# Kernel optimization log

Hardware: AMD Instinct MI355X
Metric: run time of the kernel (lower is better)

Reference implementation:

```python
import jax, jax.numpy as jnp
import numpy as np

N = 4_194_304
L = 15
SLOPE = 0.01  # torch LeakyReLU default


def setup_inputs() -> dict:
    key = jax.random.key(0)
    ks = jax.random.split(key, 16)
    n = jax.random.normal
    return {
        "x": n(ks[0], (N, 2), jnp.float32),
        # scale Linear(1,1) per layer (small init keeps exp(log_scale) stable)
        "scale_w": n(ks[1], (L, 1, 1), jnp.float32) * 0.2,
        "scale_b": n(ks[2], (L, 1), jnp.float32) * 0.1,
        # g_theta_scale: 1->32->16->1
        "sW1": n(ks[3], (L, 1, 32), jnp.float32) * 0.5,
        "sb1": n(ks[4], (L, 32), jnp.float32) * 0.1,
        "sW2": n(ks[5], (L, 32, 16), jnp.float32) * 0.2,
        "sb2": n(ks[6], (L, 16), jnp.float32) * 0.1,
        "sW3": n(ks[7], (L, 16, 1), jnp.float32) * 0.2,
        "sb3": n(ks[8], (L, 1), jnp.float32) * 0.1,
        # g_theta_shift: 1->32->16->1
        "tW1": n(ks[9], (L, 1, 32), jnp.float32) * 0.5,
        "tb1": n(ks[10], (L, 32), jnp.float32) * 0.1,
        "tW2": n(ks[11], (L, 32, 16), jnp.float32) * 0.2,
        "tb2": n(ks[12], (L, 16), jnp.float32) * 0.1,
        "tW3": n(ks[13], (L, 16, 1), jnp.float32) * 0.2,
        "tb3": n(ks[14], (L, 1), jnp.float32) * 0.1,
    }


def _mlp(h, W1, b1, W2, b2, W3, b3):
    h = jax.nn.leaky_relu(h @ W1 + b1, SLOPE)
    h = jax.nn.leaky_relu(h @ W2 + b2, SLOPE)
    return h @ W3 + b3


def reference(x, scale_w, scale_b, sW1, sb1, sW2, sb2, sW3, sb3,
              tW1, tb1, tW2, tb2, tW3, tb3):
    def step(carry, p):
        z1, z2, ld = carry
        sw, sb, w1, b1, w2, b2, w3, b3, u1, c1, u2, c2, u3, c3 = p
        x1, x2 = z2, z1  # swap
        log_scale = jnp.tanh(_mlp(x1, w1, b1, w2, b2, w3, b3)) @ sw + sb
        z2n = jnp.exp(log_scale) * x2 + _mlp(x1, u1, c1, u2, c2, u3, c3)
        return (x1, z2n, ld + log_scale), None

    init = (x[:, 1:2], x[:, 0:1], jnp.zeros_like(x[:, :1]))
    params = (scale_w, scale_b, sW1, sb1, sW2, sb2, sW3, sb3,
              tW1, tb1, tW2, tb2, tW3, tb3)
    (z1, z2, ld), _ = jax.lax.scan(step, init, params)
    return jnp.concatenate((z1, z2), axis=1), ld
```

## Files before the change

kernel.cpp:

```cpp
#include <hip/hip_runtime.h>
#include <math.h>

#define SLOPE 0.01f
#define NLAYER 15
#define FINE_CELLS 512
#define COARSE_CELLS 128
#define CELLS 640
#define FINE_NODES 513
#define NODES_PER_NET 642
#define INV_LN2 1.4426950408889634f
#define LN2F 0.6931471805599453f
#define TPB 512
#define PAIRS 4

__device__ __forceinline__ float fast_exp2(float x) {
#if __has_builtin(__builtin_amdgcn_exp2f)
    return __builtin_amdgcn_exp2f(x);
#else
    return __expf(x * LN2F);
#endif
}

__device__ __forceinline__ float mlp_exact(
    float x1,
    const float* __restrict__ W1, const float* __restrict__ b1,
    const float* __restrict__ W2, const float* __restrict__ b2,
    const float* __restrict__ W3, float b3)
{
    float h2[16];
#pragma unroll
    for (int n = 0; n < 16; ++n) h2[n] = b2[n];
#pragma unroll 2
    for (int j = 0; j < 32; ++j) {
        float h = fmaf(W1[j], x1, b1[j]);
        h = fmaxf(h, SLOPE * h);
#pragma unroll
        for (int n = 0; n < 16; ++n) h2[n] = fmaf(h, W2[j * 16 + n], h2[n]);
    }
    float o = b3;
#pragma unroll
    for (int n = 0; n < 16; ++n) {
        float h = fmaxf(h2[n], SLOPE * h2[n]);
        o = fmaf(h, W3[n], o);
    }
    return o;
}

__global__ __launch_bounds__(640) void build_tables(
    const float* __restrict__ scale_w, const float* __restrict__ scale_b,
    const float* __restrict__ sW1, const float* __restrict__ sb1,
    const float* __restrict__ sW2, const float* __restrict__ sb2,
    const float* __restrict__ sW3, const float* __restrict__ sb3,
    const float* __restrict__ tW1, const float* __restrict__ tb1,
    const float* __restrict__ tW2, const float* __restrict__ tb2,
    const float* __restrict__ tW3, const float* __restrict__ tb3,
    float* __restrict__ ws)
{
    const int m = blockIdx.x;
    const int l = m >> 1;
    const int which = m & 1;
    const float* W1 = (which ? tW1 : sW1) + l * 32;
    const float* b1 = (which ? tb1 : sb1) + l * 32;
    const float* W2 = (which ? tW2 : sW2) + l * 512;
    const float* b2 = (which ? tb2 : sb2) + l * 16;
    const float* W3 = (which ? tW3 : sW3) + l * 16;
    const float  b3 = which ? tb3[l] : sb3[l];

    __shared__ float nodes[NODES_PER_NET];

    for (int i = threadIdx.x; i < NODES_PER_NET; i += blockDim.x) {
        const float x = (i < FINE_NODES) ? (-2.0f + (float)i * (1.0f / 128.0f))
                                         : (-32.0f + (float)(i - FINE_NODES) * 0.5f);
        float o = mlp_exact(x, W1, b1, W2, b2, W3, b3);
        nodes[i] = which ? o : fmaf(tanhf(o), scale_w[l], scale_b[l]) * INV_LN2;
    }
    __syncthreads();

    for (int c = threadIdx.x; c < CELLS; c += blockDim.x) {
        int base; float x_lo, invh;
        if (c < FINE_CELLS) { base = c;     x_lo = -2.0f  + (float)c * (1.0f / 128.0f); invh = 128.0f; }
        else                { base = c + 1; x_lo = -32.0f + (float)(c - FINE_CELLS) * 0.5f; invh = 2.0f; }
        float lo = nodes[base], hi = nodes[base + 1];
        float slope = (hi - lo) * invh;
        float icpt  = fmaf(-slope, x_lo, lo);
        *(float2*)(ws + ((size_t)(l * CELLS + c) * 4) + which * 2) = make_float2(slope, icpt);
    }
}

__device__ __forceinline__ int cell_index(float x) {
    float uf = fmaf(x, 128.0f, 256.0f);
    float uc = fmaf(x, 2.0f, 576.0f);
    bool fine = (fabsf(x) < 2.0f);
    float fu = fine ? floorf(uf)
                    : fminf(fmaxf(floorf(uc), 512.0f), 639.0f);
    return (int)fu;
}

__device__ __forceinline__ void couple(const float4* __restrict__ T,
                                       float& z1, float& z2, float& ld)
{
    float4 c = T[cell_index(z2)];
    float ls = fmaf(c.x, z2, c.y);
    float g  = fmaf(c.z, z2, c.w);
    float z2n = fmaf(fast_exp2(ls), z1, g);
    z1 = z2; z2 = z2n; ld += ls;
}

__global__ __launch_bounds__(TPB) void flow_lut(
    const float4* __restrict__ x,
    const float4* __restrict__ ws,
    float4* __restrict__ out_z,
    float2* __restrict__ out_ld,
    int npair)
{
    __shared__ __align__(16) float4 buf[2][CELLS];
    const int nthreads = gridDim.x * blockDim.x;
    const int tid0 = blockIdx.x * blockDim.x + threadIdx.x;

    for (int i = threadIdx.x; i < CELLS; i += TPB) buf[0][i] = ws[i];

    float az1[PAIRS], az2[PAIRS], ald[PAIRS];
    float bz1[PAIRS], bz2[PAIRS], bld[PAIRS];
#pragma unroll
    for (int k = 0; k < PAIRS; ++k) {
        int p = tid0 + k * nthreads;
        float4 xi = (p < npair) ? x[p] : make_float4(0.f, 0.f, 0.f, 0.f);
        az1[k] = xi.y; az2[k] = xi.x; ald[k] = 0.f;
        bz1[k] = xi.w; bz2[k] = xi.z; bld[k] = 0.f;
    }
    __syncthreads();

#pragma unroll
    for (int l = 0; l < NLAYER; ++l) {
        if (l + 1 < NLAYER) {
            const float4* src = ws + (size_t)(l + 1) * CELLS;
            for (int i = threadIdx.x; i < CELLS; i += TPB)
                buf[(l + 1) & 1][i] = src[i];
        }
        const float4* T = buf[l & 1];
#pragma unroll
        for (int k = 0; k < PAIRS; ++k) {
            couple(T, az1[k], az2[k], ald[k]);
            couple(T, bz1[k], bz2[k], bld[k]);
        }
        __syncthreads();
    }

#pragma unroll
    for (int k = 0; k < PAIRS; ++k) {
        int p = tid0 + k * nthreads;
        if (p < npair) {
            out_z[p]  = make_float4(az1[k], az2[k], bz1[k], bz2[k]);
            out_ld[p] = make_float2(ald[k] * LN2F, bld[k] * LN2F);
        }
    }
}

extern "C" void kernel_launch(void* const* d_in, const int* in_sizes, int n_in,
                              void* d_out, int out_size, void* d_ws, size_t ws_size,
                              hipStream_t stream) {
    const int n = in_sizes[0] / 2;
    const int npair = n / 2;

    const float4* x       = (const float4*)d_in[0];
    const float*  scale_w = (const float*)d_in[1];
    const float*  scale_b = (const float*)d_in[2];
    const float*  sW1     = (const float*)d_in[3];
    const float*  sb1     = (const float*)d_in[4];
    const float*  sW2     = (const float*)d_in[5];
    const float*  sb2     = (const float*)d_in[6];
    const float*  sW3     = (const float*)d_in[7];
    const float*  sb3     = (const float*)d_in[8];
    const float*  tW1     = (const float*)d_in[9];
    const float*  tb1     = (const float*)d_in[10];
    const float*  tW2     = (const float*)d_in[11];
    const float*  tb2     = (const float*)d_in[12];
    const float*  tW3     = (const float*)d_in[13];
    const float*  tb3     = (const float*)d_in[14];

    float4* out_z  = (float4*)d_out;
    float2* out_ld = (float2*)((float*)d_out + (size_t)2 * n);

    build_tables<<<30, 640, 0, stream>>>(scale_w, scale_b,
        sW1, sb1, sW2, sb2, sW3, sb3,
        tW1, tb1, tW2, tb2, tW3, tb3, (float*)d_ws);

    const int nblocks = (npair + TPB * PAIRS - 1) / (TPB * PAIRS);
    flow_lut<<<nblocks, TPB, 0, stream>>>(x, (const float4*)d_ws, out_z, out_ld, npair);
}
```

Baseline: 180.2 us.

## Cache all layer tables in LDS once per persistent block

The per-layer double-buffered LUT streaming is replaced by one load of all 15 layer tables (about 150KB) into LDS per block. The kernel becomes a persistent grid of 256 blocks with 1024 threads, and each thread walks pairs with a grid-stride loop. This removes repeated global and L2 table reloads across a thousand blocks and the per-layer barriers. In exchange, occupancy is limited to one block per CU and each thread now has only two independent dependency chains instead of eight. The cell index computation also switches from floor to integer truncation, which is safe here because the fine path is non-negative and the coarse path is clamped.

```diff
diff --git a/kernel.cpp b/kernel.cpp
--- a/kernel.cpp
+++ b/kernel.cpp
@@ -8,10 +8,9 @@
 #define CELLS 640
 #define FINE_NODES 513
 #define NODES_PER_NET 642
+#define TABLE_FLOAT4 (NLAYER * CELLS)
 #define INV_LN2 1.4426950408889634f
 #define LN2F 0.6931471805599453f
-#define TPB 512
-#define PAIRS 4
 
 __device__ __forceinline__ float fast_exp2(float x) {
 #if __has_builtin(__builtin_amdgcn_exp2f)
@@ -91,9 +90,8 @@
     float uf = fmaf(x, 128.0f, 256.0f);
     float uc = fmaf(x, 2.0f, 576.0f);
     bool fine = (fabsf(x) < 2.0f);
-    float fu = fine ? floorf(uf)
-                    : fminf(fmaxf(floorf(uc), 512.0f), 639.0f);
-    return (int)fu;
+    int ic = min(max((int)uc, 512), 639);
+    return fine ? (int)uf : ic;
 }
 
 __device__ __forceinline__ void couple(const float4* __restrict__ T,
@@ -106,53 +104,30 @@
     z1 = z2; z2 = z2n; ld += ls;
 }
 
-__global__ __launch_bounds__(TPB) void flow_lut(
+__global__ __launch_bounds__(1024) void flow_lut(
     const float4* __restrict__ x,
     const float4* __restrict__ ws,
     float4* __restrict__ out_z,
     float2* __restrict__ out_ld,
     int npair)
 {
-    __shared__ __align__(16) float4 buf[2][CELLS];
-    const int nthreads = gridDim.x * blockDim.x;
-    const int tid0 = blockIdx.x * blockDim.x + threadIdx.x;
-
-    for (int i = threadIdx.x; i < CELLS; i += TPB) buf[0][i] = ws[i];
-
-    float az1[PAIRS], az2[PAIRS], ald[PAIRS];
-    float bz1[PAIRS], bz2[PAIRS], bld[PAIRS];
-#pragma unroll
-    for (int k = 0; k < PAIRS; ++k) {
-        int p = tid0 + k * nthreads;
-        float4 xi = (p < npair) ? x[p] : make_float4(0.f, 0.f, 0.f, 0.f);
-        az1[k] = xi.y; az2[k] = xi.x; ald[k] = 0.f;
-        bz1[k] = xi.w; bz2[k] = xi.z; bld[k] = 0.f;
-    }
+    __shared__ __align__(16) float4 lds[TABLE_FLOAT4];
+    for (int i = threadIdx.x; i < TABLE_FLOAT4; i += blockDim.x) lds[i] = ws[i];
     __syncthreads();
 
+    const int stride = gridDim.x * blockDim.x;
+    for (int p = blockIdx.x * blockDim.x + threadIdx.x; p < npair; p += stride) {
+        float4 xi = x[p];
+        float az1 = xi.y, az2 = xi.x, ald = 0.0f;
+        float bz1 = xi.w, bz2 = xi.z, bld = 0.0f;
 #pragma unroll
-    for (int l = 0; l < NLAYER; ++l) {
-        if (l + 1 < NLAYER) {
-            const float4* src = ws + (size_t)(l + 1) * CELLS;
-            for (int i = threadIdx.x; i < CELLS; i += TPB)
-                buf[(l + 1) & 1][i] = src[i];
+        for (int l = 0; l < NLAYER; ++l) {
+            const float4* T = lds + l * CELLS;
+            couple(T, az1, az2, ald);
+            couple(T, bz1, bz2, bld);
         }
-        const float4* T = buf[l & 1];
-#pragma unroll
-        for (int k = 0; k < PAIRS; ++k) {
-            couple(T, az1[k], az2[k], ald[k]);
-            couple(T, bz1[k], bz2[k], bld[k]);
-        }
-        __syncthreads();
-    }
-
-#pragma unroll
-    for (int k = 0; k < PAIRS; ++k) {
-        int p = tid0 + k * nthreads;
-        if (p < npair) {
-            out_z[p]  = make_float4(az1[k], az2[k], bz1[k], bz2[k]);
-            out_ld[p] = make_float2(ald[k] * LN2F, bld[k] * LN2F);
-        }
+        out_z[p]  = make_float4(az1, az2, bz1, bz2);
+        out_ld[p] = make_float2(ald * LN2F, bld * LN2F);
     }
 }
 
@@ -185,6 +160,5 @@
         sW1, sb1, sW2, sb2, sW3, sb3,
         tW1, tb1, tW2, tb2, tW3, tb3, (float*)d_ws);
 
-    const int nblocks = (npair + TPB * PAIRS - 1) / (TPB * PAIRS);
-    flow_lut<<<nblocks, TPB, 0, stream>>>(x, (const float4*)d_ws, out_z, out_ld, npair);
+    flow_lut<<<256, 1024, 0, stream>>>(x, (const float4*)d_ws, out_z, out_ld, npair);
 }
```

Measured after the change: 148.7 us. -17.5%, faster.
